# Kernel tuning notes

Measured on AMD Instinct MI355X. Metric: run time of the kernel, lower is better.

## Reference

```python
import jax, jax.numpy as jnp
import numpy as np

N_NODES = 100000
N_EDGES = 1600000
IN_SIZE = 512
HID_SIZE = 256
OUT_SIZE = 16
DROP_P = 0.5


def _degrees(idx, n):
    d = jax.ops.segment_sum(jnp.ones(idx.shape[0], jnp.float32), idx, num_segments=n)
    return jnp.maximum(d, 1.0)  # DGL clamps zero degrees to 1


def graph_conv(src, dst, feat, W, b, activation=None):
    # DGL GraphConv, norm='both': D_in^{-1/2} A D_out^{-1/2} X W + b
    n = feat.shape[0]
    inv_sqrt_dout = _degrees(src, n) ** -0.5   # out-degree of source nodes
    inv_sqrt_din = _degrees(dst, n) ** -0.5    # in-degree of destination nodes
    h = feat * inv_sqrt_dout[:, None]
    h = h @ W  # in_feats >= out_feats -> transform before aggregation (same math)
    # message passing: scatter-add source messages to destinations
    h = jax.ops.segment_sum(h[src], dst, num_segments=n)
    h = h * inv_sqrt_din[:, None] + b
    if activation is not None:
        h = activation(h)
    return h


def setup_inputs() -> dict:
    key = jax.random.key(0)
    ks = jax.random.split(key, 9)
    features = jax.random.normal(ks[0], (N_NODES, IN_SIZE), jnp.float32)
    src = jax.random.randint(ks[1], (N_EDGES,), 0, N_NODES)
    dst = jax.random.randint(ks[2], (N_EDGES,), 0, N_NODES)
    W1 = jax.random.normal(ks[3], (IN_SIZE, HID_SIZE), jnp.float32) / np.sqrt(IN_SIZE).astype(np.float32)
    b1 = jnp.zeros((HID_SIZE,), jnp.float32)
    W2 = jax.random.normal(ks[4], (HID_SIZE, HID_SIZE), jnp.float32) / np.sqrt(HID_SIZE).astype(np.float32)
    b2 = jnp.zeros((HID_SIZE,), jnp.float32)
    W3 = jax.random.normal(ks[5], (HID_SIZE, OUT_SIZE), jnp.float32) / np.sqrt(HID_SIZE).astype(np.float32)
    b3 = jnp.zeros((OUT_SIZE,), jnp.float32)
    return {"features": features, "src": src, "dst": dst,
            "W1": W1, "b1": b1, "W2": W2, "b2": b2, "W3": W3, "b3": b3}


def reference(features, src, dst, W1, b1, W2, b2, W3, b3):
    # layer 0: GraphConv + relu
    h = graph_conv(src, dst, features, W1, b1, activation=jax.nn.relu)
    # dropout(0.5) before layer 1 (deterministic fixed-key mask, training semantics)
    keep = jax.random.bernoulli(jax.random.key(42), 1.0 - DROP_P, h.shape)
    h = jnp.where(keep, h / (1.0 - DROP_P), 0.0)
    # layer 1: GraphConv (no activation)
    h = graph_conv(src, dst, h, W2, b2, activation=None)
    # layer 2: plain Linear head
    return h @ W3 + b3
```

## Files before the change

kernel.cpp:

```cpp
#include <hip/hip_runtime.h>
#include <stdint.h>

#define NN    100000
#define NE    1600000
#define IN_F  512
#define HID   256
#define OUTF  16
#define NPAD  100096
#define NBK   391
#define EPB   8192

typedef unsigned int u32;
typedef __bf16 bfrag  __attribute__((ext_vector_type(8)));
typedef float  f32x4  __attribute__((ext_vector_type(4)));
typedef short  s16x8  __attribute__((ext_vector_type(8)));

__device__ __forceinline__ u32 rotl32(u32 x, int r){ return (x<<r)|(x>>(32-r)); }

__device__ __forceinline__ bool drop_keep(u32 i){
    const u32 ks0 = 0u, ks1 = 42u, ks2 = 0x1BD11BDAu ^ 0u ^ 42u;
    u32 x0 = 0u + ks0;
    u32 x1 = i  + ks1;
#define TFR(r) { x0 += x1; x1 = rotl32(x1,(r)); x1 ^= x0; }
    TFR(13) TFR(15) TFR(26) TFR(6)   x0 += ks1; x1 += ks2 + 1u;
    TFR(17) TFR(29) TFR(16) TFR(24)  x0 += ks2; x1 += ks0 + 2u;
    TFR(13) TFR(15) TFR(26) TFR(6)   x0 += ks0; x1 += ks1 + 3u;
    TFR(17) TFR(29) TFR(16) TFR(24)  x0 += ks1; x1 += ks2 + 4u;
    TFR(13) TFR(15) TFR(26) TFR(6)   x0 += ks2; x1 += ks0 + 5u;
#undef TFR
    return ((x0 ^ x1) >> 31) == 0u;
}

__device__ __forceinline__ short f2b(float f){
    union { float f; u32 u; } v; v.f = f;
    u32 r = (v.u + 0x7FFFu + ((v.u >> 16) & 1u)) >> 16;
    return (short)r;
}
__device__ __forceinline__ float blo(u32 u){ union{u32 u; float f;} v; v.u = u << 16;         return v.f; }
__device__ __forceinline__ float bhi(u32 u){ union{u32 u; float f;} v; v.u = u & 0xFFFF0000u; return v.f; }

__device__ __forceinline__ u32 cvt_pk_bf16(float lo, float hi){
    u32 r;
    asm("v_cvt_pk_bf16_f32 %0, %1, %2" : "=v"(r) : "v"(lo), "v"(hi));
    return r;
}

__device__ __forceinline__ void gll16(const void* g, void* l){
    __builtin_amdgcn_global_load_lds((const __attribute__((address_space(1))) void*)g,
                                     (__attribute__((address_space(3))) void*)l, 16, 0, 0);
}


__global__ __launch_bounds__(256) void build_hist(const int4* __restrict__ src4,
                                                  const int4* __restrict__ dst4,
                                                  int* deg_out, int* __restrict__ bcnt){
    __shared__ int h[NBK];
    int t = threadIdx.x;
    for (int i = t; i < NBK; i += 256) h[i] = 0;
    __syncthreads();
    for (int i = blockIdx.x * 256 + t; i < NE / 4; i += gridDim.x * 256) {
        int4 s = src4[i];
        int4 d = dst4[i];
        atomicAdd(&deg_out[s.x], 1);
        atomicAdd(&deg_out[s.y], 1);
        atomicAdd(&deg_out[s.z], 1);
        atomicAdd(&deg_out[s.w], 1);
        atomicAdd(&h[d.x >> 8], 1);
        atomicAdd(&h[d.y >> 8], 1);
        atomicAdd(&h[d.z >> 8], 1);
        atomicAdd(&h[d.w >> 8], 1);
    }
    __syncthreads();
    for (int i = t; i < NBK; i += 256)
        if (h[i]) atomicAdd(&bcnt[i], h[i]);
}

__global__ __launch_bounds__(256) void finalize_deg(const int* __restrict__ deg_out,
                                                    const int* __restrict__ row_ptr,
                                                    float* isdo, float* isdi){
    int i = blockIdx.x * blockDim.x + threadIdx.x;
    if (i < NN) {
        isdo[i] = rsqrtf(fmaxf((float)deg_out[i], 1.0f));
        isdi[i] = rsqrtf(fmaxf((float)(row_ptr[i + 1] - row_ptr[i]), 1.0f));
    }
}

__global__ __launch_bounds__(512) void bucket_scan(const int* __restrict__ bcnt,
                                                   int* __restrict__ bbase,
                                                   int* __restrict__ bcur,
                                                   int* __restrict__ row_ptr){
    __shared__ int sh[512];
    int t = threadIdx.x;
    int v = (t < NBK) ? bcnt[t] : 0;
    sh[t] = v;
    __syncthreads();
    for (int off = 1; off < 512; off <<= 1) {
        int a = (t >= off) ? sh[t - off] : 0;
        __syncthreads();
        sh[t] += a;
        __syncthreads();
    }
    int excl = sh[t] - v;
    if (t < NBK) { bbase[t] = excl; bcur[t] = excl; }
    if (t == 0)  { bbase[NBK] = NE; row_ptr[NN] = NE; }
}

__global__ __launch_bounds__(256) void bucket_scatter(const int* __restrict__ src,
                                                      const int* __restrict__ dst,
                                                      int* bcur, u32* __restrict__ tmp){
    __shared__ int lh[NBK];
    __shared__ int lb[NBK];
    int t = threadIdx.x;
    for (int i = t; i < NBK; i += 256) lh[i] = 0;
    __syncthreads();
    const int e0 = blockIdx.x * EPB;
    for (int k = t * 4; k < EPB; k += 1024) {
        int e = e0 + k;
        if (e < NE) {
            int4 d = *(const int4*)(dst + e);
            atomicAdd(&lh[d.x >> 8], 1);
            atomicAdd(&lh[d.y >> 8], 1);
            atomicAdd(&lh[d.z >> 8], 1);
            atomicAdd(&lh[d.w >> 8], 1);
        }
    }
    __syncthreads();
    for (int i = t; i < NBK; i += 256) {
        int c = lh[i];
        if (c) lb[i] = atomicAdd(&bcur[i], c);
        lh[i] = 0;
    }
    __syncthreads();
    for (int k = t * 4; k < EPB; k += 1024) {
        int e = e0 + k;
        if (e < NE) {
            int4 d = *(const int4*)(dst + e);
            int4 s = *(const int4*)(src + e);
            int b0 = d.x >> 8, b1 = d.y >> 8, b2 = d.z >> 8, b3 = d.w >> 8;
            int r0 = atomicAdd(&lh[b0], 1);
            tmp[lb[b0] + r0] = ((u32)s.x << 8) | ((u32)d.x & 255u);
            int r1 = atomicAdd(&lh[b1], 1);
            tmp[lb[b1] + r1] = ((u32)s.y << 8) | ((u32)d.y & 255u);
            int r2 = atomicAdd(&lh[b2], 1);
            tmp[lb[b2] + r2] = ((u32)s.z << 8) | ((u32)d.z & 255u);
            int r3 = atomicAdd(&lh[b3], 1);
            tmp[lb[b3] + r3] = ((u32)s.w << 8) | ((u32)d.w & 255u);
        }
    }
}

__global__ __launch_bounds__(256) void bucket_finalize(const u32* __restrict__ tmp,
                                                       const int* __restrict__ bbase,
                                                       int* __restrict__ row_ptr,
                                                       int* __restrict__ col_src){
    __shared__ int h[256];
    __shared__ int wtot[4];
    const int t = threadIdx.x;
    const int b = blockIdx.x;
    const int base = bbase[b];
    const int cnt  = bbase[b + 1] - base;
    h[t] = 0;
    __syncthreads();
    for (int k = t; k < cnt; k += 256)
        atomicAdd(&h[tmp[base + k] & 255u], 1);
    __syncthreads();
    int v = h[t];
    int lane = t & 63, w = t >> 6;
    int s = v;
    #pragma unroll
    for (int off = 1; off < 64; off <<= 1) {
        int u = __shfl_up(s, off);
        if (lane >= off) s += u;
    }
    if (lane == 63) wtot[w] = s;
    __syncthreads();
    int woff = 0;
    #pragma unroll
    for (int i = 0; i < 4; ++i) woff += (i < w) ? wtot[i] : 0;
    int excl = woff + s - v;
    int d = (b << 8) + t;
    if (d < NN) row_ptr[d] = base + excl;
    h[t] = excl;
    __syncthreads();
    for (int k = t; k < cnt; k += 256) {
        u32 p = tmp[base + k];
        int r = atomicAdd(&h[p & 255u], 1);
        col_src[base + r] = (int)(p >> 8);
    }
}


template<int Kd, int Nd>
__global__ __launch_bounds__(256) void convert_wt(const float* __restrict__ W,
                                                  short* __restrict__ WT){
    int i = blockIdx.x * 256 + threadIdx.x;
    if (i >= Kd * Nd) return;
    int n = i / Kd, k = i - n * Kd;
    WT[i] = f2b(W[(size_t)k * Nd + n]);
}

__global__ __launch_bounds__(256) void gemm_x(const float* __restrict__ X,
                                              const short* __restrict__ BT,
                                              const float* __restrict__ isdo,
                                              short* __restrict__ C){
    __shared__ short As[4096];
    __shared__ short Bs[4096];

    const int t = threadIdx.x;
    const int wave = t >> 6, lane = t & 63;
    const int bm = blockIdx.x * 128;
    const int bn = blockIdx.y * 128;

    const int arow = t >> 1;
    const int kh   = t & 1;
    const bool rv  = (bm + arow) < NN;
    const float* px = X + (size_t)(bm + arow) * IN_F + kh * 16;
    short* wA = As + ((kh * 2) * 128 + arow) * 8;

    const int ch0 = wave * 128 + lane;
    const int ch1 = ch0 + 64;
    const int kb0 = ch0 >> 7, r0 = ch0 & 127;
    const int kb1 = ch1 >> 7, r1 = ch1 & 127;
    const short* pb0 = BT + (size_t)(bn + r0) * IN_F + kb0 * 8;
    const short* pb1 = BT + (size_t)(bn + r1) * IN_F + kb1 * 8;
    short* lB0 = Bs + (size_t)(wave * 128) * 8;
    short* lB1 = Bs + (size_t)(wave * 128 + 64) * 8;

    const int wr = (wave >> 1) * 64, wc = (wave & 1) * 64;
    const short* fa = As + (size_t)((lane >> 4) * 128 + wr + (lane & 15)) * 8;
    const short* fb = Bs + (size_t)((lane >> 4) * 128 + wc + (lane & 15)) * 8;

    f32x4 acc[4][4];
    #pragma unroll
    for (int m = 0; m < 4; ++m)
        #pragma unroll
        for (int n = 0; n < 4; ++n) acc[m][n] = (f32x4)0.0f;

    for (int k0 = 0; k0 < IN_F; k0 += 32) {
        gll16(pb0 + k0, lB0);
        gll16(pb1 + k0, lB1);

        float4 x0, x1, x2, x3;
        if (rv) {
            const float4* p4 = (const float4*)(px + k0);
            x0 = p4[0]; x1 = p4[1]; x2 = p4[2]; x3 = p4[3];
        } else {
            x0 = x1 = x2 = x3 = make_float4(0.f, 0.f, 0.f, 0.f);
        }
        u32 q0 = cvt_pk_bf16(x0.x, x0.y), q1 = cvt_pk_bf16(x0.z, x0.w);
        u32 q2 = cvt_pk_bf16(x1.x, x1.y), q3 = cvt_pk_bf16(x1.z, x1.w);
        u32 q4 = cvt_pk_bf16(x2.x, x2.y), q5 = cvt_pk_bf16(x2.z, x2.w);
        u32 q6 = cvt_pk_bf16(x3.x, x3.y), q7 = cvt_pk_bf16(x3.z, x3.w);
        *(uint4*)(wA)        = make_uint4(q0, q1, q2, q3);
        *(uint4*)(wA + 1024) = make_uint4(q4, q5, q6, q7);
        __syncthreads();

        bfrag af[4], bfg[4];
        #pragma unroll
        for (int m = 0; m < 4; ++m) af[m]  = *(const bfrag*)(fa + m * 128);
        #pragma unroll
        for (int n = 0; n < 4; ++n) bfg[n] = *(const bfrag*)(fb + n * 128);
        #pragma unroll
        for (int m = 0; m < 4; ++m)
            #pragma unroll
            for (int n = 0; n < 4; ++n)
                acc[m][n] = __builtin_amdgcn_mfma_f32_16x16x32_bf16(af[m], bfg[n], acc[m][n], 0, 0, 0);
        __syncthreads();
    }

    const int crow0 = bm + wr + (lane >> 4) * 4;
    const int ccol0 = bn + wc + (lane & 15);
    #pragma unroll
    for (int m = 0; m < 4; ++m)
        #pragma unroll
        for (int r = 0; r < 4; ++r) {
            int row = crow0 + m * 16 + r;
            float sc = (row < NN) ? isdo[row] : 0.0f;
            #pragma unroll
            for (int n = 0; n < 4; ++n)
                C[(size_t)row * HID + ccol0 + n * 16] = f2b(acc[m][n][r] * sc);
        }
}

template<int K>
__global__ __launch_bounds__(256) void gemm_bt(const short* __restrict__ A,
                                               const short* __restrict__ BT,
                                               short* __restrict__ C){
    __shared__ short As[4096];
    __shared__ short Bs[4096];

    const int t = threadIdx.x;
    const int wave = t >> 6, lane = t & 63;
    const int bm = blockIdx.x * 128;
    const int bn = blockIdx.y * 128;

    const int ch0 = wave * 128 + lane;
    const int ch1 = ch0 + 64;
    const int kb0 = ch0 >> 7, r0 = ch0 & 127;
    const int kb1 = ch1 >> 7, r1 = ch1 & 127;
    const short* pa0 = A  + (size_t)(bm + r0) * K + kb0 * 8;
    const short* pa1 = A  + (size_t)(bm + r1) * K + kb1 * 8;
    const short* pb0 = BT + (size_t)(bn + r0) * K + kb0 * 8;
    const short* pb1 = BT + (size_t)(bn + r1) * K + kb1 * 8;
    short* lA0 = As + (size_t)(wave * 128) * 8;
    short* lA1 = As + (size_t)(wave * 128 + 64) * 8;
    short* lB0 = Bs + (size_t)(wave * 128) * 8;
    short* lB1 = Bs + (size_t)(wave * 128 + 64) * 8;

    const int wr = (wave >> 1) * 64, wc = (wave & 1) * 64;
    const short* fa = As + (size_t)((lane >> 4) * 128 + wr + (lane & 15)) * 8;
    const short* fb = Bs + (size_t)((lane >> 4) * 128 + wc + (lane & 15)) * 8;

    f32x4 acc[4][4];
    #pragma unroll
    for (int m = 0; m < 4; ++m)
        #pragma unroll
        for (int n = 0; n < 4; ++n) acc[m][n] = (f32x4)0.0f;

    for (int k0 = 0; k0 < K; k0 += 32) {
        gll16(pa0 + k0, lA0);
        gll16(pa1 + k0, lA1);
        gll16(pb0 + k0, lB0);
        gll16(pb1 + k0, lB1);
        __syncthreads();

        bfrag af[4], bfg[4];
        #pragma unroll
        for (int m = 0; m < 4; ++m) af[m]  = *(const bfrag*)(fa + m * 128);
        #pragma unroll
        for (int n = 0; n < 4; ++n) bfg[n] = *(const bfrag*)(fb + n * 128);
        #pragma unroll
        for (int m = 0; m < 4; ++m)
            #pragma unroll
            for (int n = 0; n < 4; ++n)
                acc[m][n] = __builtin_amdgcn_mfma_f32_16x16x32_bf16(af[m], bfg[n], acc[m][n], 0, 0, 0);
        __syncthreads();
    }

    const int crow0 = bm + wr + (lane >> 4) * 4;
    const int ccol0 = bn + wc + (lane & 15);
    #pragma unroll
    for (int m = 0; m < 4; ++m)
        #pragma unroll
        for (int n = 0; n < 4; ++n)
            #pragma unroll
            for (int r = 0; r < 4; ++r)
                C[(size_t)(crow0 + m * 16 + r) * HID + ccol0 + n * 16] = f2b(acc[m][n][r]);
}

template<int MODE>
__global__ __launch_bounds__(256) void gather_agg(const short* __restrict__ H,
                                                  const int* __restrict__ rp,
                                                  const int* __restrict__ cs,
                                                  const float* __restrict__ isdi,
                                                  const float* __restrict__ isdo,
                                                  const float* __restrict__ bias,
                                                  short* __restrict__ out){
    const int lane = threadIdx.x & 63;
    const int node = __builtin_amdgcn_readfirstlane((int)(blockIdx.x * 4) + (int)(threadIdx.x >> 6));
    const int e0  = rp[node];
    const int end = rp[node + 1];
    const int sub = lane & 31, half = lane >> 5;
    const u32 off16 = (u32)sub * 16u;
    const char* Hb = (const char*)H;

    float a[8] = {0,0,0,0,0,0,0,0};
    float b[8] = {0,0,0,0,0,0,0,0};

#define LD4(s) (*(const uint4*)(Hb + ((((u32)(s)) << 9) | off16)))
#define ACC(A, u) { A[0]+=blo(u.x); A[1]+=bhi(u.x); A[2]+=blo(u.y); A[3]+=bhi(u.y); \
                    A[4]+=blo(u.z); A[5]+=bhi(u.z); A[6]+=blo(u.w); A[7]+=bhi(u.w); }

    int eb = e0;
    for (; eb + 8 <= end; eb += 8) {
        int t0 = cs[eb+0], t1 = cs[eb+1], t2 = cs[eb+2], t3 = cs[eb+3];
        int t4 = cs[eb+4], t5 = cs[eb+5], t6 = cs[eb+6], t7 = cs[eb+7];
        int s0 = half ? t1 : t0;
        int s1 = half ? t3 : t2;
        int s2 = half ? t5 : t4;
        int s3 = half ? t7 : t6;
        uint4 u0 = LD4(s0), u1 = LD4(s1), u2 = LD4(s2), u3 = LD4(s3);
        ACC(a, u0); ACC(b, u1); ACC(a, u2); ACC(b, u3);
    }
    for (; eb + 2 <= end; eb += 2) {
        int t0 = cs[eb], t1 = cs[eb+1];
        int s = half ? t1 : t0;
        uint4 u = LD4(s);
        ACC(a, u);
    }
    if (eb < end) {
        int s = cs[eb];
        uint4 u = LD4(s);
        if (half == 0) { ACC(a, u); }
    }
#undef ACC
#undef LD4
    #pragma unroll
    for (int j = 0; j < 8; ++j) a[j] += b[j];

    const int srcl = lane >> 1;
    const bool oddq = (lane & 1) != 0;
    float v[4];
    #pragma unroll
    for (int j = 0; j < 4; ++j) {
        float p0 = __shfl(a[j],     srcl);
        float p1 = __shfl(a[j + 4], srcl);
        float q0 = __shfl(a[j],     srcl + 32);
        float q1 = __shfl(a[j + 4], srcl + 32);
        v[j] = oddq ? (p1 + q1) : (p0 + q0);
    }

    float sd = isdi[node];
    float4 bb = *(const float4*)(bias + lane * 4);
    float h0 = v[0] * sd + bb.x;
    float h1 = v[1] * sd + bb.y;
    float h2 = v[2] * sd + bb.z;
    float h3 = v[3] * sd + bb.w;

    if (MODE == 0) {
        float so2 = 2.0f * isdo[node];
        u32 base = (u32)node * HID + (u32)lane * 4;
        h0 = drop_keep(base + 0) ? fmaxf(h0, 0.f) * so2 : 0.f;
        h1 = drop_keep(base + 1) ? fmaxf(h1, 0.f) * so2 : 0.f;
        h2 = drop_keep(base + 2) ? fmaxf(h2, 0.f) * so2 : 0.f;
        h3 = drop_keep(base + 3) ? fmaxf(h3, 0.f) * so2 : 0.f;
    }

    uint2 wv;
    wv.x = ((u32)(unsigned short)f2b(h1) << 16) | (u32)(unsigned short)f2b(h0);
    wv.y = ((u32)(unsigned short)f2b(h3) << 16) | (u32)(unsigned short)f2b(h2);
    *(uint2*)((char*)out + (size_t)node * 512 + (u32)lane * 8u) = wv;
}

__global__ __launch_bounds__(256) void head_kernel(const short* __restrict__ H2,
                                                   const float* __restrict__ W3,
                                                   const float* __restrict__ b3,
                                                   float* __restrict__ out){
    __shared__ float W3s[HID * OUTF];
    __shared__ short rows[16][HID + 8];
    int t = threadIdx.x;
    for (int i = t; i < HID * OUTF; i += 256) W3s[i] = W3[i];
    const int n0 = blockIdx.x * 16;
    for (int c = t; c < 16 * 32; c += 256) {
        int r = c >> 5, cc = c & 31;
        *(s16x8*)(&rows[r][cc * 8]) = *(const s16x8*)(H2 + (size_t)(n0 + r) * HID + cc * 8);
    }
    __syncthreads();
    int nl = t >> 4, k = t & 15;
    float acc = 0.0f;
    #pragma unroll 4
    for (int j = 0; j < HID; ++j)
        acc += blo((u32)(unsigned short)rows[nl][j]) * W3s[j * OUTF + k];
    out[(size_t)(n0 + nl) * OUTF + k] = acc + b3[k];
}

extern "C" void kernel_launch(void* const* d_in, const int* in_sizes, int n_in,
                              void* d_out, int out_size, void* d_ws, size_t ws_size,
                              hipStream_t stream) {
    const float* X   = (const float*)d_in[0];
    const int*   src = (const int*)  d_in[1];
    const int*   dst = (const int*)  d_in[2];
    const float* W1  = (const float*)d_in[3];
    const float* b1  = (const float*)d_in[4];
    const float* W2  = (const float*)d_in[5];
    const float* b2  = (const float*)d_in[6];
    const float* W3  = (const float*)d_in[7];
    const float* b3  = (const float*)d_in[8];
    float* out = (float*)d_out;

    char* ws = (char*)d_ws;
    size_t o = 0;
    int*   deg_out = (int*)  (ws + o); o += (size_t)NN * 4;
    int*   bcnt    = (int*)  (ws + o); o += (size_t)NBK * 4;
    float* isdo    = (float*)(ws + o); o += (size_t)NN * 4;
    float* isdi    = (float*)(ws + o); o += (size_t)NN * 4;
    int*   row_ptr = (int*)  (ws + o); o += (size_t)(NN + 1) * 4;
    int*   bbase   = (int*)  (ws + o); o += (size_t)(NBK + 1) * 4;
    int*   bcur    = (int*)  (ws + o); o += (size_t)NBK * 4;
    int*   col_src = (int*)  (ws + o); o += (size_t)NE * 4;
    o = (o + 255) & ~(size_t)255;
    short* W1t = (short*)(ws + o); o += (size_t)IN_F * HID * 2;
    short* W2t = (short*)(ws + o); o += (size_t)HID * HID * 2;
    o = (o + 255) & ~(size_t)255;
    short* hA    = (short*)(ws + o); o += (size_t)NPAD * HID * 2;
    short* hB    = (short*)(ws + o); o += (size_t)NPAD * HID * 2;
    short* h2pre = (short*)(ws + o); o += (size_t)NPAD * HID * 2;
    if (ws_size < o) return;
    short* h2  = hA;
    u32*   tmp = (u32*)hB;

    const size_t zlen = (size_t)NN * 4 + (size_t)NBK * 4;
    hipMemsetAsync(deg_out, 0, zlen, stream);

    build_hist<<<256, 256, 0, stream>>>((const int4*)src, (const int4*)dst, deg_out, bcnt);
    bucket_scan<<<1, 512, 0, stream>>>(bcnt, bbase, bcur, row_ptr);
    bucket_scatter<<<(NE + EPB - 1) / EPB, 256, 0, stream>>>(src, dst, bcur, tmp);
    bucket_finalize<<<NBK, 256, 0, stream>>>(tmp, bbase, row_ptr, col_src);
    finalize_deg<<<(NN + 255) / 256, 256, 0, stream>>>(deg_out, row_ptr, isdo, isdi);

    convert_wt<IN_F, HID><<<IN_F * HID / 256, 256, 0, stream>>>(W1, W1t);
    convert_wt<HID, HID><<<HID * HID / 256, 256, 0, stream>>>(W2, W2t);

    dim3 ggrid(NPAD / 128, 2);

    gemm_x<<<ggrid, 256, 0, stream>>>(X, W1t, isdo, hA);
    gather_agg<0><<<NN / 4, 256, 0, stream>>>(hA, row_ptr, col_src, isdi, isdo, b1, hB);

    gemm_bt<HID><<<ggrid, 256, 0, stream>>>(hB, W2t, h2pre);
    gather_agg<1><<<NN / 4, 256, 0, stream>>>(h2pre, row_ptr, col_src, isdi, isdo, b2, h2);

    head_kernel<<<NN / 16, 256, 0, stream>>>(h2, W3, b3, out);
}
```

Before: 535.7 us.

## Load fp32 X tiles via direct-to-LDS loads and deepen aggregation unroll

New measurement: 535.7 us. Within noise of the previous version (+0.0%).

```diff
diff --git a/kernel.cpp b/kernel.cpp
--- a/kernel.cpp
+++ b/kernel.cpp
@@ -203,19 +203,22 @@
                                               const short* __restrict__ BT,
                                               const float* __restrict__ isdo,
                                               short* __restrict__ C){
-    __shared__ short As[4096];
-    __shared__ short Bs[4096];
+    __shared__ __align__(16) float As[4096];
+    __shared__ __align__(16) short Bs[4096];
 
     const int t = threadIdx.x;
     const int wave = t >> 6, lane = t & 63;
     const int bm = blockIdx.x * 128;
     const int bn = blockIdx.y * 128;
 
-    const int arow = t >> 1;
-    const int kh   = t & 1;
-    const bool rv  = (bm + arow) < NN;
-    const float* px = X + (size_t)(bm + arow) * IN_F + kh * 16;
-    short* wA = As + ((kh * 2) * 128 + arow) * 8;
+    const int gsw = lane ^ ((lane >> 3) & 7);
+    const int rl  = gsw >> 1;
+    const int pp  = gsw & 1;
+    const float* pa0 = X + (size_t)(((bm + 0*32 + rl) < NN) ? (bm + 0*32 + rl) : 0) * IN_F + wave * 8 + pp * 4;
+    const float* pa1 = X + (size_t)(((bm + 1*32 + rl) < NN) ? (bm + 1*32 + rl) : 0) * IN_F + wave * 8 + pp * 4;
+    const float* pa2 = X + (size_t)(((bm + 2*32 + rl) < NN) ? (bm + 2*32 + rl) : 0) * IN_F + wave * 8 + pp * 4;
+    const float* pa3 = X + (size_t)(((bm + 3*32 + rl) < NN) ? (bm + 3*32 + rl) : 0) * IN_F + wave * 8 + pp * 4;
+    float* lA = As + wave * 1024;
 
     const int ch0 = wave * 128 + lane;
     const int ch1 = ch0 + 64;
@@ -227,8 +230,8 @@
     short* lB1 = Bs + (size_t)(wave * 128 + 64) * 8;
 
     const int wr = (wave >> 1) * 64, wc = (wave & 1) * 64;
-    const short* fa = As + (size_t)((lane >> 4) * 128 + wr + (lane & 15)) * 8;
-    const short* fb = Bs + (size_t)((lane >> 4) * 128 + wc + (lane & 15)) * 8;
+    const int kq = lane >> 4, r15 = lane & 15;
+    const short* fb = Bs + (size_t)(kq * 128 + wc + r15) * 8;
 
     f32x4 acc[4][4];
     #pragma unroll
@@ -237,27 +240,30 @@
         for (int n = 0; n < 4; ++n) acc[m][n] = (f32x4)0.0f;
 
     for (int k0 = 0; k0 < IN_F; k0 += 32) {
+        gll16(pa0 + k0, lA);
+        gll16(pa1 + k0, lA + 256);
+        gll16(pa2 + k0, lA + 512);
+        gll16(pa3 + k0, lA + 768);
         gll16(pb0 + k0, lB0);
         gll16(pb1 + k0, lB1);
-
-        float4 x0, x1, x2, x3;
-        if (rv) {
-            const float4* p4 = (const float4*)(px + k0);
-            x0 = p4[0]; x1 = p4[1]; x2 = p4[2]; x3 = p4[3];
-        } else {
-            x0 = x1 = x2 = x3 = make_float4(0.f, 0.f, 0.f, 0.f);
+        __syncthreads();
+
+        bfrag af[4], bfg[4];
+        #pragma unroll
+        for (int m = 0; m < 4; ++m) {
+            int r  = wr + m * 16 + r15;
+            int j  = r >> 5, rr = r & 31;
+            int g0 = 2 * rr;
+            int G0 = g0 ^ ((g0 >> 3) & 7);
+            int g1 = g0 + 1;
+            int G1 = g1 ^ ((g1 >> 3) & 7);
+            const float* base = As + kq * 1024 + j * 256;
+            float4 f0 = *(const float4*)(base + G0 * 4);
+            float4 f1 = *(const float4*)(base + G1 * 4);
+            uint4 q = make_uint4(cvt_pk_bf16(f0.x, f0.y), cvt_pk_bf16(f0.z, f0.w),
+                                 cvt_pk_bf16(f1.x, f1.y), cvt_pk_bf16(f1.z, f1.w));
+            af[m] = *(bfrag*)&q;
         }
-        u32 q0 = cvt_pk_bf16(x0.x, x0.y), q1 = cvt_pk_bf16(x0.z, x0.w);
-        u32 q2 = cvt_pk_bf16(x1.x, x1.y), q3 = cvt_pk_bf16(x1.z, x1.w);
-        u32 q4 = cvt_pk_bf16(x2.x, x2.y), q5 = cvt_pk_bf16(x2.z, x2.w);
-        u32 q6 = cvt_pk_bf16(x3.x, x3.y), q7 = cvt_pk_bf16(x3.z, x3.w);
-        *(uint4*)(wA)        = make_uint4(q0, q1, q2, q3);
-        *(uint4*)(wA + 1024) = make_uint4(q4, q5, q6, q7);
-        __syncthreads();
-
-        bfrag af[4], bfg[4];
-        #pragma unroll
-        for (int m = 0; m < 4; ++m) af[m]  = *(const bfrag*)(fa + m * 128);
         #pragma unroll
         for (int n = 0; n < 4; ++n) bfg[n] = *(const bfrag*)(fb + n * 128);
         #pragma unroll
@@ -286,8 +292,8 @@
 __global__ __launch_bounds__(256) void gemm_bt(const short* __restrict__ A,
                                                const short* __restrict__ BT,
                                                short* __restrict__ C){
-    __shared__ short As[4096];
-    __shared__ short Bs[4096];
+    __shared__ __align__(16) short As[4096];
+    __shared__ __align__(16) short Bs[4096];
 
     const int t = threadIdx.x;
     const int wave = t >> 6, lane = t & 63;
@@ -372,6 +378,24 @@
                     A[4]+=blo(u.z); A[5]+=bhi(u.z); A[6]+=blo(u.w); A[7]+=bhi(u.w); }
 
     int eb = e0;
+    for (; eb + 16 <= end; eb += 16) {
+        int t0 = cs[eb+0],  t1 = cs[eb+1],  t2 = cs[eb+2],  t3 = cs[eb+3];
+        int t4 = cs[eb+4],  t5 = cs[eb+5],  t6 = cs[eb+6],  t7 = cs[eb+7];
+        int t8 = cs[eb+8],  t9 = cs[eb+9],  tA = cs[eb+10], tB = cs[eb+11];
+        int tC = cs[eb+12], tD = cs[eb+13], tE = cs[eb+14], tF = cs[eb+15];
+        int s0 = half ? t1 : t0;
+        int s1 = half ? t3 : t2;
+        int s2 = half ? t5 : t4;
+        int s3 = half ? t7 : t6;
+        int s4 = half ? t9 : t8;
+        int s5 = half ? tB : tA;
+        int s6 = half ? tD : tC;
+        int s7 = half ? tF : tE;
+        uint4 u0 = LD4(s0), u1 = LD4(s1), u2 = LD4(s2), u3 = LD4(s3);
+        uint4 u4 = LD4(s4), u5 = LD4(s5), u6 = LD4(s6), u7 = LD4(s7);
+        ACC(a, u0); ACC(b, u1); ACC(a, u2); ACC(b, u3);
+        ACC(a, u4); ACC(b, u5); ACC(a, u6); ACC(b, u7);
+    }
     for (; eb + 8 <= end; eb += 8) {
         int t0 = cs[eb+0], t1 = cs[eb+1], t2 = cs[eb+2], t3 = cs[eb+3];
         int t4 = cs[eb+4], t5 = cs[eb+5], t6 = cs[eb+6], t7 = cs[eb+7];
```
